# Performance work log

Measured on AMD Instinct MI355X. Metric: run time of the kernel, lower is better.

The kernel has to match this reference:

```python
import jax, jax.numpy as jnp
import numpy as np

BN_EPS = 1e-5
CHEB_K = 9


def laplacian(x, A):
    # x: [B,N,F_in], A: [B,N,N]
    diff = x[:, None, :, :] - x[:, :, None, :]            # [B,N,N,F]
    dist = jnp.sqrt(jnp.sum(diff * diff, axis=-1))        # [B,N,N]
    W = A / (dist + 0.001)
    d = 1.0 / jnp.sqrt(jnp.sum(W, axis=1))                # [B,N]
    I = jnp.eye(W.shape[1], dtype=W.dtype)[None]
    L = I - d[:, :, None] * W * d[:, None, :]             # sym-normalized
    L = L / 2 - I
    return L


def cheb_conv(L, x, W, b):
    # Chebyshev recursion, k=9: T0=x, T1=Lx, Tk = 2 L T(k-1) - T(k-2)
    Ts = [x, jnp.matmul(L, x)]
    for _ in range(CHEB_K - 2):
        Ts.append(2.0 * jnp.matmul(L, Ts[-1]) - Ts[-2])
    xt = jnp.concatenate(Ts, axis=-1)                     # [B,N,F_in*k]
    return jnp.matmul(xt, W) + b


def batchnorm_train(x, gamma, beta):
    # x: [B,N,C]; BatchNorm1d over flattened B*N rows (train mode, biased var)
    B, N, C = x.shape
    xf = x.reshape(B * N, C)
    mu = jnp.mean(xf, axis=0)
    var = jnp.mean((xf - mu) ** 2, axis=0)
    xn = (xf - mu) / jnp.sqrt(var + BN_EPS)
    return (xn * gamma + beta).reshape(B, N, C)


def setup_inputs() -> dict:
    key = jax.random.key(0)
    ks = jax.random.split(key, 12)
    B, N = 32, 1024
    x = jax.random.normal(ks[0], (B, N, 3), dtype=jnp.float32)
    A = jax.random.uniform(ks[1], (B, N, N), dtype=jnp.float32)
    def lin(k, fin, fout):
        return jax.random.normal(k, (fin, fout), dtype=jnp.float32) / np.sqrt(fin)
    return {
        "x": x, "A": A,
        "W1": lin(ks[2], 3 * CHEB_K, 32), "b1": jnp.zeros((32,), jnp.float32),
        "g1": jnp.ones((32,), jnp.float32), "be1": jnp.zeros((32,), jnp.float32),
        "W2": lin(ks[3], 32 * CHEB_K, 64), "b2": jnp.zeros((64,), jnp.float32),
        "g2": jnp.ones((64,), jnp.float32), "be2": jnp.zeros((64,), jnp.float32),
        "W3": lin(ks[4], 64 * CHEB_K, 64), "b3": jnp.zeros((64,), jnp.float32),
        "g3": jnp.ones((64,), jnp.float32), "be3": jnp.zeros((64,), jnp.float32),
        "Wfc": lin(ks[5], 64, 1), "bfc": jnp.zeros((1,), jnp.float32),
    }


def reference(x, A, W1, b1, g1, be1, W2, b2, g2, be2, W3, b3, g3, be3, Wfc, bfc):
    L = jax.lax.stop_gradient(laplacian(x, A))  # .detach() in original
    h = cheb_conv(L, x, W1, b1)
    h = jax.nn.elu(batchnorm_train(h, g1, be1))
    h = cheb_conv(L, h, W2, b2)
    h = jax.nn.elu(batchnorm_train(h, g2, be2))
    h = cheb_conv(L, h, W3, b3)
    h = jax.nn.elu(batchnorm_train(h, g3, be3))
    h = jnp.mean(h, axis=1)                     # [B,64]
    return jnp.matmul(h, Wfc) + bfc             # [B,1]
```

## Files before the change

kernel.cpp:

```cpp
#include <hip/hip_runtime.h>
#include <hip/hip_bf16.h>
#include <math.h>

constexpr int NN = 1024;
constexpr int NB = 32;
constexpr int ROWS = NB * NN;
constexpr int NSLICE = 8;

using f32x4 = __attribute__((ext_vector_type(4))) float;
using s16x8 = __attribute__((ext_vector_type(8))) short;
using us8 = __attribute__((ext_vector_type(8))) unsigned short;

__device__ inline unsigned short f2bf(float f) {
  unsigned u = __float_as_uint(f);
  unsigned r = (u + 0x7FFFu + ((u >> 16) & 1u)) >> 16;
  return (unsigned short)r;
}
__device__ inline float bf2f(unsigned short h) {
  return __uint_as_float((unsigned)h << 16);
}

__global__ __launch_bounds__(256) void colsum_w(float* __restrict__ A,
                                                const float* __restrict__ x,
                                                float* __restrict__ S) {
  const int b = blockIdx.z;
  const int j = blockIdx.x * 256 + threadIdx.x;
  const int slice = blockIdx.y;
  const int ibase = slice * 128;
  __shared__ float xs[128 * 3];
  for (int idx = threadIdx.x; idx < 384; idx += 256)
    xs[idx] = x[(size_t)(b * NN + ibase) * 3 + idx];
  const float xj0 = x[(size_t)(b * NN + j) * 3 + 0];
  const float xj1 = x[(size_t)(b * NN + j) * 3 + 1];
  const float xj2 = x[(size_t)(b * NN + j) * 3 + 2];
  __syncthreads();
  float s = 0.f;
  size_t off = ((size_t)b << 20) + (size_t)ibase * NN + j;
  for (int ii = 0; ii < 128; ++ii, off += NN) {
    float a = A[off];
    float dx = xj0 - xs[ii * 3 + 0];
    float dy = xj1 - xs[ii * 3 + 1];
    float dz = xj2 - xs[ii * 3 + 2];
    float dist = sqrtf(dx * dx + dy * dy + dz * dz);
    float w = a / (dist + 0.001f);
    A[off] = w;
    s += w;
  }
  S[(size_t)slice * ROWS + b * NN + j] = s;
}

__global__ __launch_bounds__(256) void d_kernel(const float* __restrict__ S,
                                                float* __restrict__ D) {
  int i = blockIdx.x * 256 + threadIdx.x;
  if (i < ROWS) {
    float s = 0.f;
#pragma unroll
    for (int p = 0; p < NSLICE; ++p) s += S[(size_t)p * ROWS + i];
    D[i] = 1.f / sqrtf(s);
  }
}

__global__ __launch_bounds__(256) void pack_L(float* __restrict__ A,
                                              const float* __restrict__ D,
                                              unsigned short* __restrict__ Lh,
                                              unsigned short* __restrict__ Ll) {
  const int b = blockIdx.y;
  const int rb = blockIdx.x;
  const int i0 = rb * 16;
  const float* Db = &D[b * NN];
  for (int ci = threadIdx.x; ci < 2048; ci += 256) {
    int kt = ci >> 6, l = ci & 63;
    int r = l & 15, kg = l >> 4;
    int i = i0 + r;
    int j0 = kt * 32 + kg * 8;
    size_t ga = ((size_t)b << 20) + (size_t)i * NN + j0;
    float4 w0 = *reinterpret_cast<const float4*>(&A[ga]);
    float4 w1 = *reinterpret_cast<const float4*>(&A[ga + 4]);
    float di = Db[i];
    float4 d0 = *reinterpret_cast<const float4*>(&Db[j0]);
    float4 d1 = *reinterpret_cast<const float4*>(&Db[j0 + 4]);
    float lv[8];
    lv[0] = -0.5f * di * d0.x * w0.x;
    lv[1] = -0.5f * di * d0.y * w0.y;
    lv[2] = -0.5f * di * d0.z * w0.z;
    lv[3] = -0.5f * di * d0.w * w0.w;
    lv[4] = -0.5f * di * d1.x * w1.x;
    lv[5] = -0.5f * di * d1.y * w1.y;
    lv[6] = -0.5f * di * d1.z * w1.z;
    lv[7] = -0.5f * di * d1.w * w1.w;
    int dd = i - j0;
    if (dd >= 0 && dd < 8) lv[dd] -= 0.5f;
    float4 o0 = {lv[0], lv[1], lv[2], lv[3]};
    float4 o1 = {lv[4], lv[5], lv[6], lv[7]};
    *reinterpret_cast<float4*>(&A[ga]) = o0;
    *reinterpret_cast<float4*>(&A[ga + 4]) = o1;
    us8 vh, vl;
#pragma unroll
    for (int jj = 0; jj < 8; ++jj) {
      unsigned short hi = f2bf(lv[jj]);
      vh[jj] = hi;
      vl[jj] = f2bf(lv[jj] - bf2f(hi));
    }
    size_t po = (((size_t)b * 64 + rb) * 32 + kt) * 512 + (size_t)l * 8;
    *reinterpret_cast<us8*>(&Lh[po]) = vh;
    *reinterpret_cast<us8*>(&Ll[po]) = vl;
  }
}

__global__ __launch_bounds__(256) void scale_L(float* __restrict__ A,
                                               const float* __restrict__ D) {
  const long total4 = (long)NB * NN * NN / 4;
  for (long idx = (long)blockIdx.x * 256 + threadIdx.x; idx < total4;
       idx += (long)gridDim.x * 256) {
    long base = idx * 4;
    int j0 = (int)(base & (NN - 1));
    int i = (int)((base >> 10) & (NN - 1));
    int b = (int)(base >> 20);
    float4 w = reinterpret_cast<float4*>(A)[idx];
    float di = D[b * NN + i];
    float4 dj = *reinterpret_cast<const float4*>(&D[b * NN + j0]);
    float4 l;
    l.x = -0.5f * di * dj.x * w.x;
    l.y = -0.5f * di * dj.y * w.y;
    l.z = -0.5f * di * dj.z * w.z;
    l.w = -0.5f * di * dj.w * w.w;
    int dd = i - j0;
    if (dd == 0) l.x -= 0.5f;
    else if (dd == 1) l.y -= 0.5f;
    else if (dd == 2) l.z -= 0.5f;
    else if (dd == 3) l.w -= 0.5f;
    reinterpret_cast<float4*>(A)[idx] = l;
  }
}

template <int F, int G>
__global__ __launch_bounds__(256) void acc0_gemm(const float* __restrict__ h,
                                                 const float* __restrict__ W0,
                                                 float* __restrict__ acc) {
  constexpr int RB = 64;
  constexpr int TGN = G / 16;
  __shared__ float Hs[RB][F + 1];
  __shared__ float Ws[F][G];
  const int tid = threadIdx.x;
  const size_t row0 = (size_t)blockIdx.x * RB;
  for (int idx = tid; idx < RB * F; idx += 256)
    Hs[idx / F][idx % F] = h[row0 * F + idx];
  for (int idx = tid; idx < F * G; idx += 256)
    Ws[idx / G][idx % G] = W0[idx];
  __syncthreads();
  const int tx = tid % 16, ty = tid / 16;
  float o[4][TGN];
#pragma unroll
  for (int r = 0; r < 4; ++r)
#pragma unroll
    for (int c = 0; c < TGN; ++c) o[r][c] = 0.f;
#pragma unroll 4
  for (int f = 0; f < F; ++f) {
    float a[4];
#pragma unroll
    for (int r = 0; r < 4; ++r) a[r] = Hs[ty * 4 + r][f];
#pragma unroll
    for (int c = 0; c < TGN; ++c) {
      float w = Ws[f][tx * TGN + c];
#pragma unroll
      for (int r = 0; r < 4; ++r) o[r][c] = fmaf(a[r], w, o[r][c]);
    }
  }
#pragma unroll
  for (int r = 0; r < 4; ++r) {
    size_t base = (row0 + ty * 4 + r) * G + tx * TGN;
#pragma unroll
    for (int c = 0; c < TGN; ++c) acc[base + c] = o[r][c];
  }
}

__global__ __launch_bounds__(256) void cheb_l1(
    const float* __restrict__ Lg, const float* __restrict__ Tprev,
    const float* __restrict__ Tpp, float* __restrict__ Tk,
    const float* __restrict__ Wk, float* __restrict__ acc, float alpha,
    float beta) {
  __shared__ float Ts[NN * 3];
  __shared__ float tkv[16][4];
  const int b = blockIdx.y;
  const int i0 = blockIdx.x * 16;
  const int tid = threadIdx.x;
  const float* tpb = &Tprev[(size_t)b * NN * 3];
  for (int idx = tid; idx < 768; idx += 256)
    *reinterpret_cast<float4*>(&Ts[idx * 4]) =
        *reinterpret_cast<const float4*>(&tpb[idx * 4]);
  __syncthreads();
  const int wv = tid >> 6, ln = tid & 63;
#pragma unroll
  for (int r = 0; r < 4; ++r) {
    const int i = i0 + wv * 4 + r;
    const float* Lrow = &Lg[((size_t)b << 20) + (size_t)i * NN];
    float a0 = 0.f, a1 = 0.f, a2 = 0.f;
#pragma unroll
    for (int c = 0; c < 16; ++c) {
      int j = c * 64 + ln;
      float w = Lrow[j];
      a0 = fmaf(w, Ts[j * 3 + 0], a0);
      a1 = fmaf(w, Ts[j * 3 + 1], a1);
      a2 = fmaf(w, Ts[j * 3 + 2], a2);
    }
#pragma unroll
    for (int off = 32; off; off >>= 1) {
      a0 += __shfl_down(a0, off, 64);
      a1 += __shfl_down(a1, off, 64);
      a2 += __shfl_down(a2, off, 64);
    }
    if (ln == 0) {
      const size_t rbase = (size_t)(b * NN + i) * 3;
      float t0 = alpha * a0, t1 = alpha * a1, t2 = alpha * a2;
      if (beta != 0.f) {
        t0 = fmaf(beta, Tpp[rbase + 0], t0);
        t1 = fmaf(beta, Tpp[rbase + 1], t1);
        t2 = fmaf(beta, Tpp[rbase + 2], t2);
      }
      Tk[rbase + 0] = t0;
      Tk[rbase + 1] = t1;
      Tk[rbase + 2] = t2;
      tkv[wv * 4 + r][0] = t0;
      tkv[wv * 4 + r][1] = t1;
      tkv[wv * 4 + r][2] = t2;
    }
  }
  __syncthreads();
  for (int idx = tid; idx < 16 * 32; idx += 256) {
    int rr = idx >> 5, cc = idx & 31;
    float v = tkv[rr][0] * Wk[cc] + tkv[rr][1] * Wk[32 + cc] +
              tkv[rr][2] * Wk[64 + cc];
    acc[(size_t)(b * NN + i0 + rr) * 32 + cc] += v;
  }
}

template <int FT>
__global__ __launch_bounds__(256) void pack_T(const float* __restrict__ h,
                                              unsigned short* __restrict__ Oh,
                                              unsigned short* __restrict__ Ol) {
  constexpr int F = FT * 16;
  __shared__ float Ts[64][F + 1];
  const int b = blockIdx.y;
  const int m0 = blockIdx.x * 64;
  const int tid = threadIdx.x;
  for (int idx = tid; idx < 64 * (F / 4); idx += 256) {
    int row = idx / (F / 4), c4 = idx % (F / 4);
    float4 v = *reinterpret_cast<const float4*>(
        &h[((size_t)(b * NN + m0 + row)) * F + c4 * 4]);
    Ts[row][c4 * 4 + 0] = v.x;
    Ts[row][c4 * 4 + 1] = v.y;
    Ts[row][c4 * 4 + 2] = v.z;
    Ts[row][c4 * 4 + 3] = v.w;
  }
  __syncthreads();
  for (int ci = tid; ci < 8 * F; ci += 256) {
    int nc = ci / F, f = ci % F;
    int n0 = nc * 8;
    us8 vh, vl;
#pragma unroll
    for (int j = 0; j < 8; ++j) {
      float t = Ts[n0 + j][f];
      unsigned short hi = f2bf(t);
      vh[j] = hi;
      vl[j] = f2bf(t - bf2f(hi));
    }
    int gn = m0 + n0;
    int kt = gn >> 5, kg = (gn >> 3) & 3;
    size_t off = (((size_t)b * FT + (f >> 4)) * 32 + kt) * 512 +
                 (size_t)(kg * 16 + (f & 15)) * 8;
    *reinterpret_cast<us8*>(&Oh[off]) = vh;
    *reinterpret_cast<us8*>(&Ol[off]) = vl;
  }
}

template <int FT, int G>
__global__ __launch_bounds__(256) void cheb_mfma_p(
    const unsigned short* __restrict__ Lh, const unsigned short* __restrict__ Ll,
    const unsigned short* __restrict__ Bh, const unsigned short* __restrict__ Bl,
    const float* __restrict__ Tpp, float* __restrict__ Tk,
    unsigned short* __restrict__ Oh, unsigned short* __restrict__ Ol,
    const float* __restrict__ Wk, float* __restrict__ acc, float alpha,
    float beta) {
  constexpr int F = FT * 16;
  constexpr int TGN = G / 16;
  __shared__ float Ts[64][F + 1];
  __shared__ float Ws[F][G];
  const int tid = threadIdx.x;

  int id = blockIdx.x;
  int xcd = id & 7, t2 = id >> 3;
  int mt = t2 & 15;
  int b = xcd + 8 * (t2 >> 4);
  const int m0 = mt * 64;

  for (int idx = tid; idx < F * G / 4; idx += 256) {
    int r = idx / (G / 4), c4 = idx % (G / 4);
    *reinterpret_cast<float4*>(&Ws[r][c4 * 4]) =
        *reinterpret_cast<const float4*>(&Wk[r * G + c4 * 4]);
  }

  const int wv = tid >> 6, l = tid & 63;
  const size_t lane8 = (size_t)l * 8;
  const size_t Abase = (((size_t)b * 64 + mt * 4 + wv) * 32) * 512 + lane8;
  const size_t Bbase = (((size_t)b * FT) * 32) * 512 + lane8;

  f32x4 av[FT];
#pragma unroll
  for (int c = 0; c < FT; ++c) av[c] = {0.f, 0.f, 0.f, 0.f};

#pragma unroll 2
  for (int kt = 0; kt < 32; ++kt) {
    s16x8 a_h, a_l, b_h[FT], b_l[FT];
    size_t aoff = Abase + (size_t)kt * 512;
    a_h = *reinterpret_cast<const s16x8*>(&Lh[aoff]);
    a_l = *reinterpret_cast<const s16x8*>(&Ll[aoff]);
#pragma unroll
    for (int c = 0; c < FT; ++c) {
      size_t off = Bbase + ((size_t)c * 32 + kt) * 512;
      b_h[c] = *reinterpret_cast<const s16x8*>(&Bh[off]);
      b_l[c] = *reinterpret_cast<const s16x8*>(&Bl[off]);
    }
#pragma unroll
    for (int c = 0; c < FT; ++c) {
      av[c] = __builtin_amdgcn_mfma_f32_16x16x32_bf16(a_h, b_h[c], av[c], 0, 0, 0);
      av[c] = __builtin_amdgcn_mfma_f32_16x16x32_bf16(a_l, b_h[c], av[c], 0, 0, 0);
      av[c] = __builtin_amdgcn_mfma_f32_16x16x32_bf16(a_h, b_l[c], av[c], 0, 0, 0);
      av[c] = __builtin_amdgcn_mfma_f32_16x16x32_bf16(a_l, b_l[c], av[c], 0, 0, 0);
    }
  }

  const int kg = l >> 4, fr = l & 15;
#pragma unroll
  for (int c = 0; c < FT; ++c)
#pragma unroll
    for (int r = 0; r < 4; ++r)
      Ts[wv * 16 + kg * 4 + r][c * 16 + fr] = av[c][r];
  __syncthreads();

  const bool hasB = (beta != 0.f);
  for (int idx = tid; idx < 64 * (F / 4); idx += 256) {
    int row = idx / (F / 4), f0 = (idx % (F / 4)) * 4;
    size_t g = ((size_t)(b * NN + m0 + row)) * F + f0;
    float t0 = alpha * Ts[row][f0 + 0];
    float t1 = alpha * Ts[row][f0 + 1];
    float t2 = alpha * Ts[row][f0 + 2];
    float t3 = alpha * Ts[row][f0 + 3];
    if (hasB) {
      float4 p = *reinterpret_cast<const float4*>(&Tpp[g]);
      t0 = fmaf(beta, p.x, t0);
      t1 = fmaf(beta, p.y, t1);
      t2 = fmaf(beta, p.z, t2);
      t3 = fmaf(beta, p.w, t3);
    }
    float4 tv = {t0, t1, t2, t3};
    *reinterpret_cast<float4*>(&Tk[g]) = tv;
    Ts[row][f0 + 0] = t0;
    Ts[row][f0 + 1] = t1;
    Ts[row][f0 + 2] = t2;
    Ts[row][f0 + 3] = t3;
  }
  __syncthreads();

  for (int ci = tid; ci < 8 * F; ci += 256) {
    int nc = ci / F, f = ci % F;
    int n0 = nc * 8;
    us8 vh, vl;
#pragma unroll
    for (int j = 0; j < 8; ++j) {
      float t = Ts[n0 + j][f];
      unsigned short hi = f2bf(t);
      vh[j] = hi;
      vl[j] = f2bf(t - bf2f(hi));
    }
    int gn = m0 + n0;
    int kt = gn >> 5, kgo = (gn >> 3) & 3;
    size_t off = (((size_t)b * FT + (f >> 4)) * 32 + kt) * 512 +
                 (size_t)(kgo * 16 + (f & 15)) * 8;
    *reinterpret_cast<us8*>(&Oh[off]) = vh;
    *reinterpret_cast<us8*>(&Ol[off]) = vl;
  }

  const int tx = tid & 15, ty = tid >> 4;
  float o[4][TGN];
#pragma unroll
  for (int r = 0; r < 4; ++r)
#pragma unroll
    for (int c = 0; c < TGN; ++c) o[r][c] = 0.f;
#pragma unroll 8
  for (int f = 0; f < F; ++f) {
    float a[4];
#pragma unroll
    for (int r = 0; r < 4; ++r) a[r] = Ts[ty * 4 + r][f];
#pragma unroll
    for (int c = 0; c < TGN; ++c) {
      float w = Ws[f][tx * TGN + c];
#pragma unroll
      for (int r = 0; r < 4; ++r) o[r][c] = fmaf(a[r], w, o[r][c]);
    }
  }
#pragma unroll
  for (int r = 0; r < 4; ++r) {
    size_t base = ((size_t)(b * NN + m0 + ty * 4 + r)) * G + tx * TGN;
    float4 v = *reinterpret_cast<const float4*>(&acc[base]);
    v.x += o[r][0];
    v.y += o[r][1];
    v.z += o[r][2];
    v.w += o[r][3];
    *reinterpret_cast<float4*>(&acc[base]) = v;
  }
}

template <int BM, int F, int G>
__global__ __launch_bounds__(256) void cheb_gemm(
    const float* __restrict__ Lg, const float* __restrict__ Tprev,
    const float* __restrict__ Tpp, float* __restrict__ Tk,
    const float* __restrict__ Wk, float* __restrict__ acc, float alpha,
    float beta) {
  constexpr int BK = 32;
  constexpr int TM = 4, TN = 4;
  constexpr int NTX = F / TN;
  constexpr int NTY = BM / TM;
  static_assert(NTX * NTY == 256, "tile mismatch");
  constexpr int TGN = G / NTX;

  __shared__ float As[BM][BK + 1];
  __shared__ float Bs[BK][F];
  __shared__ float Ws[F][G];
  __shared__ float Ts[BM][F + 1];

  const int tid = threadIdx.x;
  const int tx = tid % NTX, ty = tid / NTX;
  const int b = blockIdx.y;
  const int i0 = blockIdx.x * BM;

  constexpr int W_ITERS = (F * G / 4) / 256;
#pragma unroll
  for (int it = 0; it < W_ITERS; ++it) {
    int idx = tid + it * 256;
    int r = idx / (G / 4), c4 = idx % (G / 4);
    float4 v = *reinterpret_cast<const float4*>(&Wk[r * G + c4 * 4]);
    *reinterpret_cast<float4*>(&Ws[r][c4 * 4]) = v;
  }

  float accT[TM][TN];
#pragma unroll
  for (int r = 0; r < TM; ++r)
#pragma unroll
    for (int c = 0; c < TN; ++c) accT[r][c] = 0.f;

  const size_t Lbase = ((size_t)b << 20);
  constexpr int A_ITERS = (BM * (BK / 4)) / 256;
  constexpr int B_ITERS = (BK * (F / 4) + 255) / 256;

  for (int k0 = 0; k0 < NN; k0 += BK) {
#pragma unroll
    for (int it = 0; it < A_ITERS; ++it) {
      int idx = tid + it * 256;
      int m = idx >> 3, k4 = idx & 7;
      float4 v = *reinterpret_cast<const float4*>(
          &Lg[Lbase + (size_t)(i0 + m) * NN + k0 + k4 * 4]);
      As[m][k4 * 4 + 0] = v.x;
      As[m][k4 * 4 + 1] = v.y;
      As[m][k4 * 4 + 2] = v.z;
      As[m][k4 * 4 + 3] = v.w;
    }
#pragma unroll
    for (int it = 0; it < B_ITERS; ++it) {
      int idx = tid + it * 256;
      int kr = idx / (F / 4), c4 = idx % (F / 4);
      float4 v = *reinterpret_cast<const float4*>(
          &Tprev[(size_t)(b * NN + k0 + kr) * F + c4 * 4]);
      *reinterpret_cast<float4*>(&Bs[kr][c4 * 4]) = v;
    }
    __syncthreads();
#pragma unroll
    for (int kk = 0; kk < BK; ++kk) {
      float a[TM];
#pragma unroll
      for (int r = 0; r < TM; ++r) a[r] = As[ty * TM + r][kk];
      float4 bv = *reinterpret_cast<const float4*>(&Bs[kk][tx * TN]);
      float bb[4] = {bv.x, bv.y, bv.z, bv.w};
#pragma unroll
      for (int r = 0; r < TM; ++r)
#pragma unroll
        for (int c = 0; c < TN; ++c)
          accT[r][c] = fmaf(a[r], bb[c], accT[r][c]);
    }
    __syncthreads();
  }

  const bool hasB = (beta != 0.f);
#pragma unroll
  for (int r = 0; r < TM; ++r) {
    int row = i0 + ty * TM + r;
    size_t gidx = (size_t)(b * NN + row) * F + tx * TN;
    float t0 = alpha * accT[r][0], t1 = alpha * accT[r][1];
    float t2 = alpha * accT[r][2], t3 = alpha * accT[r][3];
    if (hasB) {
      float4 p = *reinterpret_cast<const float4*>(&Tpp[gidx]);
      t0 = fmaf(beta, p.x, t0);
      t1 = fmaf(beta, p.y, t1);
      t2 = fmaf(beta, p.z, t2);
      t3 = fmaf(beta, p.w, t3);
    }
    float4 tv = {t0, t1, t2, t3};
    *reinterpret_cast<float4*>(&Tk[gidx]) = tv;
    Ts[ty * TM + r][tx * TN + 0] = t0;
    Ts[ty * TM + r][tx * TN + 1] = t1;
    Ts[ty * TM + r][tx * TN + 2] = t2;
    Ts[ty * TM + r][tx * TN + 3] = t3;
  }
  __syncthreads();

  float oacc[TM][TGN];
#pragma unroll
  for (int r = 0; r < TM; ++r)
#pragma unroll
    for (int c = 0; c < TGN; ++c) oacc[r][c] = 0.f;
#pragma unroll 8
  for (int f = 0; f < F; ++f) {
    float a[TM];
#pragma unroll
    for (int r = 0; r < TM; ++r) a[r] = Ts[ty * TM + r][f];
#pragma unroll
    for (int c = 0; c < TGN; ++c) {
      float w = Ws[f][tx * TGN + c];
#pragma unroll
      for (int r = 0; r < TM; ++r) oacc[r][c] = fmaf(a[r], w, oacc[r][c]);
    }
  }
#pragma unroll
  for (int r = 0; r < TM; ++r) {
    int row = i0 + ty * TM + r;
    size_t base = (size_t)(b * NN + row) * G + tx * TGN;
#pragma unroll
    for (int c = 0; c < TGN; ++c) acc[base + c] += oacc[r][c];
  }
}

constexpr int BN_BLOCKS = 256;

template <int C>
__global__ __launch_bounds__(256) void bn_part(const float* __restrict__ acc,
                                               double* __restrict__ part) {
  constexpr int GR = 256 / C;
  const int tid = threadIdx.x;
  const int c = tid % C;
  const int g = tid / C;
  double s = 0.0, s2 = 0.0;
  for (int r = blockIdx.x * GR + g; r < ROWS; r += BN_BLOCKS * GR) {
    double v = (double)acc[(size_t)r * C + c];
    s += v;
    s2 += v * v;
  }
  __shared__ double Ls[256], Ls2[256];
  Ls[tid] = s;
  Ls2[tid] = s2;
  __syncthreads();
  for (int str = 128; str >= C; str >>= 1) {
    if (tid < str) {
      Ls[tid] += Ls[tid + str];
      Ls2[tid] += Ls2[tid + str];
    }
    __syncthreads();
  }
  if (tid < C) {
    part[(size_t)blockIdx.x * 2 * C + tid] = Ls[tid];
    part[(size_t)blockIdx.x * 2 * C + C + tid] = Ls2[tid];
  }
}

template <int C>
__global__ void bn_final(const double* __restrict__ part,
                         const float* __restrict__ g,
                         const float* __restrict__ be,
                         float* __restrict__ sc) {
  int t = threadIdx.x;
  if (t < C) {
    double s = 0.0, s2 = 0.0;
    for (int b = 0; b < BN_BLOCKS; ++b) {
      s += part[(size_t)b * 2 * C + t];
      s2 += part[(size_t)b * 2 * C + C + t];
    }
    double mu = s / ROWS;
    double var = s2 / ROWS - mu * mu;
    float scale = g[t] / sqrtf((float)var + 1e-5f);
    sc[t] = scale;
    sc[C + t] = be[t] - (float)mu * scale;
  }
}

template <int C>
__global__ __launch_bounds__(256) void bn_apply_elu(
    const float* __restrict__ acc, const float* __restrict__ sc,
    float* __restrict__ h) {
  const long total4 = (long)ROWS * C / 4;
  for (long idx = (long)blockIdx.x * 256 + threadIdx.x; idx < total4;
       idx += (long)gridDim.x * 256) {
    long base = idx * 4;
    int c0 = (int)(base % C);
    float4 v = reinterpret_cast<const float4*>(acc)[idx];
    float t0 = fmaf(v.x, sc[c0 + 0], sc[C + c0 + 0]);
    float t1 = fmaf(v.y, sc[c0 + 1], sc[C + c0 + 1]);
    float t2 = fmaf(v.z, sc[c0 + 2], sc[C + c0 + 2]);
    float t3 = fmaf(v.w, sc[c0 + 3], sc[C + c0 + 3]);
    float4 o;
    o.x = t0 > 0.f ? t0 : expm1f(t0);
    o.y = t1 > 0.f ? t1 : expm1f(t1);
    o.z = t2 > 0.f ? t2 : expm1f(t2);
    o.w = t3 > 0.f ? t3 : expm1f(t3);
    reinterpret_cast<float4*>(h)[idx] = o;
  }
}

__global__ __launch_bounds__(256) void final_k(const float* __restrict__ h,
                                               const float* __restrict__ Wfc,
                                               const float* __restrict__ bfc,
                                               float* __restrict__ out) {
  const int b = blockIdx.x;
  const int tid = threadIdx.x;
  const int c = tid % 64;
  const int g = tid / 64;
  float s = 0.f;
  for (int r = g; r < NN; r += 4) s += h[(size_t)(b * NN + r) * 64 + c];
  __shared__ float red[256];
  red[tid] = s;
  __syncthreads();
  if (tid < 128) red[tid] += red[tid + 128];
  __syncthreads();
  if (tid < 64) {
    float pooled = (red[tid] + red[tid + 64]) * (1.0f / 1024.0f);
    float v = pooled * Wfc[tid];
#pragma unroll
    for (int off = 32; off; off >>= 1) v += __shfl_down(v, off, 64);
    if (tid == 0) out[b] = v + bfc[0];
  }
}

extern "C" void kernel_launch(void* const* d_in, const int* in_sizes, int n_in,
                              void* d_out, int out_size, void* d_ws,
                              size_t ws_size, hipStream_t stream) {
  const float* x = (const float*)d_in[0];
  float* A = (float*)d_in[1];
  const float* W1 = (const float*)d_in[2];
  const float* g1 = (const float*)d_in[4];
  const float* be1 = (const float*)d_in[5];
  const float* W2 = (const float*)d_in[6];
  const float* g2 = (const float*)d_in[8];
  const float* be2 = (const float*)d_in[9];
  const float* W3 = (const float*)d_in[10];
  const float* g3 = (const float*)d_in[12];
  const float* be3 = (const float*)d_in[13];
  const float* Wfc = (const float*)d_in[14];
  const float* bfc = (const float*)d_in[15];

  constexpr size_t TBUF = 2097152;
  float* wsf = (float*)d_ws;
  float* buf0 = wsf;
  float* buf1 = buf0 + TBUF;
  float* buf2 = buf1 + TBUF;
  float* acc = buf2 + TBUF;
  unsigned short* tt = (unsigned short*)(wsf + 4 * TBUF);
  unsigned short* TTh[2] = {tt, tt + 2 * 2097152};
  unsigned short* TTl[2] = {tt + 2097152, tt + 3 * 2097152};
  unsigned short* Lh = (unsigned short*)(wsf + 4 * TBUF + 4194304);
  unsigned short* Ll = Lh + (size_t)NB * NN * NN;
  float* S = wsf + 4 * TBUF + 4194304 + 2 * ((size_t)NB * NN * NN / 2);
  float* D = S + (size_t)NSLICE * ROWS;
  double* part_m = (double*)(D + ROWS);
  float* sc_m = (float*)(part_m + (size_t)BN_BLOCKS * 2 * 64);
  size_t need_m = (size_t)((sc_m + 128) - wsf) * sizeof(float);

  float* S_f = wsf + 4 * TBUF;
  float* D_f = S_f + (size_t)NSLICE * ROWS;
  double* part_f = (double*)(D_f + ROWS);
  float* sc_f = (float*)(part_f + (size_t)BN_BLOCKS * 2 * 64);
  size_t need_f = (size_t)((sc_f + 128) - wsf) * sizeof(float);

  const bool use_m = (ws_size >= need_m);
  if (!use_m && ws_size < need_f) return;
  float* Sp = use_m ? S : S_f;
  float* Dp = use_m ? D : D_f;
  double* part = use_m ? part_m : part_f;
  float* sc = use_m ? sc_m : sc_f;

  float* bufs[3] = {buf0, buf1, buf2};

  colsum_w<<<dim3(4, NSLICE, NB), 256, 0, stream>>>(A, x, Sp);
  d_kernel<<<128, 256, 0, stream>>>(Sp, Dp);
  if (use_m) {
    pack_L<<<dim3(64, NB), 256, 0, stream>>>(A, Dp, Lh, Ll);
  } else {
    scale_L<<<4096, 256, 0, stream>>>(A, Dp);
  }

  acc0_gemm<3, 32><<<512, 256, 0, stream>>>(x, W1, acc);
  {
    const float* Tm1 = x;
    const float* Tm2 = nullptr;
    for (int k = 1; k <= 8; ++k) {
      float* outb = bufs[k % 3];
      float alpha = (k == 1) ? 1.f : 2.f;
      float beta = (k == 1) ? 0.f : -1.f;
      cheb_l1<<<dim3(64, NB), 256, 0, stream>>>(
          A, Tm1, (k == 1) ? x : Tm2, outb, W1 + k * 3 * 32, acc, alpha, beta);
      Tm2 = Tm1;
      Tm1 = outb;
    }
  }
  bn_part<32><<<BN_BLOCKS, 256, 0, stream>>>(acc, part);
  bn_final<32><<<1, 64, 0, stream>>>(part, g1, be1, sc);
  bn_apply_elu<32><<<1024, 256, 0, stream>>>(acc, sc, buf0);

  acc0_gemm<32, 64><<<512, 256, 0, stream>>>(buf0, W2, acc);
  if (use_m) {
    pack_T<2><<<dim3(16, NB), 256, 0, stream>>>(buf0, TTh[0], TTl[0]);
    const float* Tm1 = buf0;
    const float* Tm2 = nullptr;
    for (int k = 1; k <= 8; ++k) {
      float* outb = bufs[k % 3];
      int si = (k - 1) & 1, so = k & 1;
      float alpha = (k == 1) ? 1.f : 2.f;
      float beta = (k == 1) ? 0.f : -1.f;
      cheb_mfma_p<2, 64><<<512, 256, 0, stream>>>(
          Lh, Ll, TTh[si], TTl[si], (k == 1) ? buf0 : Tm2, outb, TTh[so],
          TTl[so], W2 + k * 32 * 64, acc, alpha, beta);
      Tm2 = Tm1;
      Tm1 = outb;
    }
  } else {
    const float* Tm1 = buf0;
    const float* Tm2 = nullptr;
    for (int k = 1; k <= 8; ++k) {
      float* outb = bufs[k % 3];
      float alpha = (k == 1) ? 1.f : 2.f;
      float beta = (k == 1) ? 0.f : -1.f;
      cheb_gemm<128, 32, 64><<<dim3(8, NB), 256, 0, stream>>>(
          A, Tm1, (k == 1) ? buf0 : Tm2, outb, W2 + k * 32 * 64, acc, alpha,
          beta);
      Tm2 = Tm1;
      Tm1 = outb;
    }
  }
  bn_part<64><<<BN_BLOCKS, 256, 0, stream>>>(acc, part);
  bn_final<64><<<1, 64, 0, stream>>>(part, g2, be2, sc);
  bn_apply_elu<64><<<2048, 256, 0, stream>>>(acc, sc, buf0);

  acc0_gemm<64, 64><<<512, 256, 0, stream>>>(buf0, W3, acc);
  if (use_m) {
    pack_T<4><<<dim3(16, NB), 256, 0, stream>>>(buf0, TTh[0], TTl[0]);
    const float* Tm1 = buf0;
    const float* Tm2 = nullptr;
    for (int k = 1; k <= 8; ++k) {
      float* outb = bufs[k % 3];
      int si = (k - 1) & 1, so = k & 1;
      float alpha = (k == 1) ? 1.f : 2.f;
      float beta = (k == 1) ? 0.f : -1.f;
      cheb_mfma_p<4, 64><<<512, 256, 0, stream>>>(
          Lh, Ll, TTh[si], TTl[si], (k == 1) ? buf0 : Tm2, outb, TTh[so],
          TTl[so], W3 + k * 64 * 64, acc, alpha, beta);
      Tm2 = Tm1;
      Tm1 = outb;
    }
  } else {
    const float* Tm1 = buf0;
    const float* Tm2 = nullptr;
    for (int k = 1; k <= 8; ++k) {
      float* outb = bufs[k % 3];
      float alpha = (k == 1) ? 1.f : 2.f;
      float beta = (k == 1) ? 0.f : -1.f;
      cheb_gemm<64, 64, 64><<<dim3(16, NB), 256, 0, stream>>>(
          A, Tm1, (k == 1) ? buf0 : Tm2, outb, W3 + k * 64 * 64, acc, alpha,
          beta);
      Tm2 = Tm1;
      Tm1 = outb;
    }
  }
  bn_part<64><<<BN_BLOCKS, 256, 0, stream>>>(acc, part);
  bn_final<64><<<1, 64, 0, stream>>>(part, g3, be3, sc);
  bn_apply_elu<64><<<2048, 256, 0, stream>>>(acc, sc, buf0);

  final_k<<<NB, 256, 0, stream>>>(buf0, Wfc, bfc, (float*)d_out);
}
```

Baseline: 1.217 ms.

## Split MFMA Chebyshev K loop across waves, drop lo*lo term, fuse L scaling into layer 1

pack_L no longer writes the scaled fp32 Laplacian back to A. The first-layer cheb_l1 kernel now applies the D scaling and identity shift on the fly from the raw weights, which removes a full 128MB write pass. The MFMA Chebyshev kernel uses 32-row tiles and splits the K dimension across two wave pairs, reduced through shared memory, and the grid doubles to 1024 blocks for more parallelism. It also drops the low*low bf16 correction MFMA, trading a little accuracy for fewer matrix instructions.

```diff
diff --git a/kernel.cpp b/kernel.cpp
--- a/kernel.cpp
+++ b/kernel.cpp
@@ -60,7 +60,7 @@
   }
 }
 
-__global__ __launch_bounds__(256) void pack_L(float* __restrict__ A,
+__global__ __launch_bounds__(256) void pack_L(const float* __restrict__ A,
                                               const float* __restrict__ D,
                                               unsigned short* __restrict__ Lh,
                                               unsigned short* __restrict__ Ll) {
@@ -90,10 +90,6 @@
     lv[7] = -0.5f * di * d1.w * w1.w;
     int dd = i - j0;
     if (dd >= 0 && dd < 8) lv[dd] -= 0.5f;
-    float4 o0 = {lv[0], lv[1], lv[2], lv[3]};
-    float4 o1 = {lv[4], lv[5], lv[6], lv[7]};
-    *reinterpret_cast<float4*>(&A[ga]) = o0;
-    *reinterpret_cast<float4*>(&A[ga + 4]) = o1;
     us8 vh, vl;
 #pragma unroll
     for (int jj = 0; jj < 8; ++jj) {
@@ -175,19 +171,26 @@
 }
 
 __global__ __launch_bounds__(256) void cheb_l1(
-    const float* __restrict__ Lg, const float* __restrict__ Tprev,
-    const float* __restrict__ Tpp, float* __restrict__ Tk,
-    const float* __restrict__ Wk, float* __restrict__ acc, float alpha,
-    float beta) {
+    const float* __restrict__ Lg, const float* __restrict__ Dv,
+    const float* __restrict__ Tprev, const float* __restrict__ Tpp,
+    float* __restrict__ Tk, const float* __restrict__ Wk,
+    float* __restrict__ acc, float alpha, float beta) {
   __shared__ float Ts[NN * 3];
+  __shared__ float ds[NN];
   __shared__ float tkv[16][4];
   const int b = blockIdx.y;
   const int i0 = blockIdx.x * 16;
   const int tid = threadIdx.x;
+  const bool fused = (Dv != nullptr);
   const float* tpb = &Tprev[(size_t)b * NN * 3];
   for (int idx = tid; idx < 768; idx += 256)
     *reinterpret_cast<float4*>(&Ts[idx * 4]) =
         *reinterpret_cast<const float4*>(&tpb[idx * 4]);
+  if (fused) {
+    for (int idx = tid; idx < 256; idx += 256)
+      *reinterpret_cast<float4*>(&ds[idx * 4]) =
+          *reinterpret_cast<const float4*>(&Dv[b * NN + idx * 4]);
+  }
   __syncthreads();
   const int wv = tid >> 6, ln = tid & 63;
 #pragma unroll
@@ -199,6 +202,7 @@
     for (int c = 0; c < 16; ++c) {
       int j = c * 64 + ln;
       float w = Lrow[j];
+      if (fused) w *= ds[j];
       a0 = fmaf(w, Ts[j * 3 + 0], a0);
       a1 = fmaf(w, Ts[j * 3 + 1], a1);
       a2 = fmaf(w, Ts[j * 3 + 2], a2);
@@ -211,7 +215,16 @@
     }
     if (ln == 0) {
       const size_t rbase = (size_t)(b * NN + i) * 3;
-      float t0 = alpha * a0, t1 = alpha * a1, t2 = alpha * a2;
+      float l0, l1, l2;
+      if (fused) {
+        float di = ds[i];
+        l0 = -0.5f * di * a0 - 0.5f * Ts[i * 3 + 0];
+        l1 = -0.5f * di * a1 - 0.5f * Ts[i * 3 + 1];
+        l2 = -0.5f * di * a2 - 0.5f * Ts[i * 3 + 2];
+      } else {
+        l0 = a0; l1 = a1; l2 = a2;
+      }
+      float t0 = alpha * l0, t1 = alpha * l1, t2 = alpha * l2;
       if (beta != 0.f) {
         t0 = fmaf(beta, Tpp[rbase + 0], t0);
         t1 = fmaf(beta, Tpp[rbase + 1], t1);
@@ -283,15 +296,15 @@
     float beta) {
   constexpr int F = FT * 16;
   constexpr int TGN = G / 16;
-  __shared__ float Ts[64][F + 1];
+  __shared__ float Ts[32][F + 1];
   __shared__ float Ws[F][G];
   const int tid = threadIdx.x;
 
   int id = blockIdx.x;
   int xcd = id & 7, t2 = id >> 3;
-  int mt = t2 & 15;
-  int b = xcd + 8 * (t2 >> 4);
-  const int m0 = mt * 64;
+  int mt = t2 & 31;
+  int b = xcd + 8 * (t2 >> 5);
+  const int m0 = mt * 32;
 
   for (int idx = tid; idx < F * G / 4; idx += 256) {
     int r = idx / (G / 4), c4 = idx % (G / 4);
@@ -300,16 +313,17 @@
   }
 
   const int wv = tid >> 6, l = tid & 63;
+  const int rt = wv >> 1, kh = wv & 1;
   const size_t lane8 = (size_t)l * 8;
-  const size_t Abase = (((size_t)b * 64 + mt * 4 + wv) * 32) * 512 + lane8;
+  const size_t Abase = (((size_t)b * 64 + mt * 2 + rt) * 32) * 512 + lane8;
   const size_t Bbase = (((size_t)b * FT) * 32) * 512 + lane8;
 
   f32x4 av[FT];
 #pragma unroll
   for (int c = 0; c < FT; ++c) av[c] = {0.f, 0.f, 0.f, 0.f};
 
-#pragma unroll 2
-  for (int kt = 0; kt < 32; ++kt) {
+  const int kt0 = kh * 16;
+  for (int kt = kt0; kt < kt0 + 16; ++kt) {
     s16x8 a_h, a_l, b_h[FT], b_l[FT];
     size_t aoff = Abase + (size_t)kt * 512;
     a_h = *reinterpret_cast<const s16x8*>(&Lh[aoff]);
@@ -325,20 +339,29 @@
       av[c] = __builtin_amdgcn_mfma_f32_16x16x32_bf16(a_h, b_h[c], av[c], 0, 0, 0);
       av[c] = __builtin_amdgcn_mfma_f32_16x16x32_bf16(a_l, b_h[c], av[c], 0, 0, 0);
       av[c] = __builtin_amdgcn_mfma_f32_16x16x32_bf16(a_h, b_l[c], av[c], 0, 0, 0);
-      av[c] = __builtin_amdgcn_mfma_f32_16x16x32_bf16(a_l, b_l[c], av[c], 0, 0, 0);
     }
   }
 
   const int kg = l >> 4, fr = l & 15;
-#pragma unroll
-  for (int c = 0; c < FT; ++c)
-#pragma unroll
-    for (int r = 0; r < 4; ++r)
-      Ts[wv * 16 + kg * 4 + r][c * 16 + fr] = av[c][r];
+  if (kh == 0) {
+#pragma unroll
+    for (int c = 0; c < FT; ++c)
+#pragma unroll
+      for (int r = 0; r < 4; ++r)
+        Ts[rt * 16 + kg * 4 + r][c * 16 + fr] = av[c][r];
+  }
+  __syncthreads();
+  if (kh == 1) {
+#pragma unroll
+    for (int c = 0; c < FT; ++c)
+#pragma unroll
+      for (int r = 0; r < 4; ++r)
+        Ts[rt * 16 + kg * 4 + r][c * 16 + fr] += av[c][r];
+  }
   __syncthreads();
 
   const bool hasB = (beta != 0.f);
-  for (int idx = tid; idx < 64 * (F / 4); idx += 256) {
+  for (int idx = tid; idx < 32 * (F / 4); idx += 256) {
     int row = idx / (F / 4), f0 = (idx % (F / 4)) * 4;
     size_t g = ((size_t)(b * NN + m0 + row)) * F + f0;
     float t0 = alpha * Ts[row][f0 + 0];
@@ -361,7 +384,7 @@
   }
   __syncthreads();
 
-  for (int ci = tid; ci < 8 * F; ci += 256) {
+  for (int ci = tid; ci < 4 * F; ci += 256) {
     int nc = ci / F, f = ci % F;
     int n0 = nc * 8;
     us8 vh, vl;
@@ -381,26 +404,25 @@
   }
 
   const int tx = tid & 15, ty = tid >> 4;
-  float o[4][TGN];
-#pragma unroll
-  for (int r = 0; r < 4; ++r)
+  float o[2][TGN];
+#pragma unroll
+  for (int r = 0; r < 2; ++r)
 #pragma unroll
     for (int c = 0; c < TGN; ++c) o[r][c] = 0.f;
 #pragma unroll 8
   for (int f = 0; f < F; ++f) {
-    float a[4];
-#pragma unroll
-    for (int r = 0; r < 4; ++r) a[r] = Ts[ty * 4 + r][f];
+    float a0 = Ts[ty * 2 + 0][f];
+    float a1 = Ts[ty * 2 + 1][f];
 #pragma unroll
     for (int c = 0; c < TGN; ++c) {
       float w = Ws[f][tx * TGN + c];
-#pragma unroll
-      for (int r = 0; r < 4; ++r) o[r][c] = fmaf(a[r], w, o[r][c]);
-    }
-  }
-#pragma unroll
-  for (int r = 0; r < 4; ++r) {
-    size_t base = ((size_t)(b * NN + m0 + ty * 4 + r)) * G + tx * TGN;
+      o[0][c] = fmaf(a0, w, o[0][c]);
+      o[1][c] = fmaf(a1, w, o[1][c]);
+    }
+  }
+#pragma unroll
+  for (int r = 0; r < 2; ++r) {
+    size_t base = ((size_t)(b * NN + m0 + ty * 2 + r)) * G + tx * TGN;
     float4 v = *reinterpret_cast<const float4*>(&acc[base]);
     v.x += o[r][0];
     v.y += o[r][1];
@@ -694,6 +716,7 @@
     scale_L<<<4096, 256, 0, stream>>>(A, Dp);
   }
 
+  const float* Dfuse = use_m ? Dp : nullptr;
   acc0_gemm<3, 32><<<512, 256, 0, stream>>>(x, W1, acc);
   {
     const float* Tm1 = x;
@@ -703,7 +726,8 @@
       float alpha = (k == 1) ? 1.f : 2.f;
       float beta = (k == 1) ? 0.f : -1.f;
       cheb_l1<<<dim3(64, NB), 256, 0, stream>>>(
-          A, Tm1, (k == 1) ? x : Tm2, outb, W1 + k * 3 * 32, acc, alpha, beta);
+          A, Dfuse, Tm1, (k == 1) ? x : Tm2, outb, W1 + k * 3 * 32, acc, alpha,
+          beta);
       Tm2 = Tm1;
       Tm1 = outb;
     }
@@ -722,7 +746,7 @@
       int si = (k - 1) & 1, so = k & 1;
       float alpha = (k == 1) ? 1.f : 2.f;
       float beta = (k == 1) ? 0.f : -1.f;
-      cheb_mfma_p<2, 64><<<512, 256, 0, stream>>>(
+      cheb_mfma_p<2, 64><<<1024, 256, 0, stream>>>(
           Lh, Ll, TTh[si], TTl[si], (k == 1) ? buf0 : Tm2, outb, TTh[so],
           TTl[so], W2 + k * 32 * 64, acc, alpha, beta);
       Tm2 = Tm1;
@@ -756,7 +780,7 @@
       int si = (k - 1) & 1, so = k & 1;
       float alpha = (k == 1) ? 1.f : 2.f;
       float beta = (k == 1) ? 0.f : -1.f;
-      cheb_mfma_p<4, 64><<<512, 256, 0, stream>>>(
+      cheb_mfma_p<4, 64><<<1024, 256, 0, stream>>>(
           Lh, Ll, TTh[si], TTl[si], (k == 1) ? buf0 : Tm2, outb, TTh[so],
           TTl[so], W3 + k * 64 * 64, acc, alpha, beta);
       Tm2 = Tm1;
```

Measured after the change: 1.332 ms. 1.1x slower.

## Skip fp32 L writeback in pack_L; apply D scaling inside cheb_l1; drop lo*lo MFMA

Applied to the files above, without the earlier changes.

pack_L no longer writes the normalized fp32 Laplacian back into A, which removes a full 128 MB store pass. In the fused path, cheb_l1 reads the unnormalized W from A and applies the D row and column scaling plus the identity term on the fly from a shared-memory copy of D. Separately, the split-bf16 MFMA product drops the lo*lo term, cutting matrix instructions by a quarter at a small cost in accuracy.

```diff
diff --git a/kernel.cpp b/kernel.cpp
--- a/kernel.cpp
+++ b/kernel.cpp
@@ -60,7 +60,7 @@
   }
 }
 
-__global__ __launch_bounds__(256) void pack_L(float* __restrict__ A,
+__global__ __launch_bounds__(256) void pack_L(const float* __restrict__ A,
                                               const float* __restrict__ D,
                                               unsigned short* __restrict__ Lh,
                                               unsigned short* __restrict__ Ll) {
@@ -90,10 +90,6 @@
     lv[7] = -0.5f * di * d1.w * w1.w;
     int dd = i - j0;
     if (dd >= 0 && dd < 8) lv[dd] -= 0.5f;
-    float4 o0 = {lv[0], lv[1], lv[2], lv[3]};
-    float4 o1 = {lv[4], lv[5], lv[6], lv[7]};
-    *reinterpret_cast<float4*>(&A[ga]) = o0;
-    *reinterpret_cast<float4*>(&A[ga + 4]) = o1;
     us8 vh, vl;
 #pragma unroll
     for (int jj = 0; jj < 8; ++jj) {
@@ -175,19 +171,26 @@
 }
 
 __global__ __launch_bounds__(256) void cheb_l1(
-    const float* __restrict__ Lg, const float* __restrict__ Tprev,
-    const float* __restrict__ Tpp, float* __restrict__ Tk,
-    const float* __restrict__ Wk, float* __restrict__ acc, float alpha,
-    float beta) {
+    const float* __restrict__ Lg, const float* __restrict__ Dv,
+    const float* __restrict__ Tprev, const float* __restrict__ Tpp,
+    float* __restrict__ Tk, const float* __restrict__ Wk,
+    float* __restrict__ acc, float alpha, float beta) {
   __shared__ float Ts[NN * 3];
+  __shared__ float ds[NN];
   __shared__ float tkv[16][4];
   const int b = blockIdx.y;
   const int i0 = blockIdx.x * 16;
   const int tid = threadIdx.x;
+  const bool fused = (Dv != nullptr);
   const float* tpb = &Tprev[(size_t)b * NN * 3];
   for (int idx = tid; idx < 768; idx += 256)
     *reinterpret_cast<float4*>(&Ts[idx * 4]) =
         *reinterpret_cast<const float4*>(&tpb[idx * 4]);
+  if (fused) {
+    for (int idx = tid; idx < 256; idx += 256)
+      *reinterpret_cast<float4*>(&ds[idx * 4]) =
+          *reinterpret_cast<const float4*>(&Dv[b * NN + idx * 4]);
+  }
   __syncthreads();
   const int wv = tid >> 6, ln = tid & 63;
 #pragma unroll
@@ -199,6 +202,7 @@
     for (int c = 0; c < 16; ++c) {
       int j = c * 64 + ln;
       float w = Lrow[j];
+      if (fused) w *= ds[j];
       a0 = fmaf(w, Ts[j * 3 + 0], a0);
       a1 = fmaf(w, Ts[j * 3 + 1], a1);
       a2 = fmaf(w, Ts[j * 3 + 2], a2);
@@ -211,7 +215,16 @@
     }
     if (ln == 0) {
       const size_t rbase = (size_t)(b * NN + i) * 3;
-      float t0 = alpha * a0, t1 = alpha * a1, t2 = alpha * a2;
+      float l0, l1, l2;
+      if (fused) {
+        float di = ds[i];
+        l0 = -0.5f * di * a0 - 0.5f * Ts[i * 3 + 0];
+        l1 = -0.5f * di * a1 - 0.5f * Ts[i * 3 + 1];
+        l2 = -0.5f * di * a2 - 0.5f * Ts[i * 3 + 2];
+      } else {
+        l0 = a0; l1 = a1; l2 = a2;
+      }
+      float t0 = alpha * l0, t1 = alpha * l1, t2 = alpha * l2;
       if (beta != 0.f) {
         t0 = fmaf(beta, Tpp[rbase + 0], t0);
         t1 = fmaf(beta, Tpp[rbase + 1], t1);
@@ -325,7 +338,6 @@
       av[c] = __builtin_amdgcn_mfma_f32_16x16x32_bf16(a_h, b_h[c], av[c], 0, 0, 0);
       av[c] = __builtin_amdgcn_mfma_f32_16x16x32_bf16(a_l, b_h[c], av[c], 0, 0, 0);
       av[c] = __builtin_amdgcn_mfma_f32_16x16x32_bf16(a_h, b_l[c], av[c], 0, 0, 0);
-      av[c] = __builtin_amdgcn_mfma_f32_16x16x32_bf16(a_l, b_l[c], av[c], 0, 0, 0);
     }
   }
 
@@ -694,6 +706,7 @@
     scale_L<<<4096, 256, 0, stream>>>(A, Dp);
   }
 
+  const float* Dfuse = use_m ? Dp : nullptr;
   acc0_gemm<3, 32><<<512, 256, 0, stream>>>(x, W1, acc);
   {
     const float* Tm1 = x;
@@ -703,7 +716,8 @@
       float alpha = (k == 1) ? 1.f : 2.f;
       float beta = (k == 1) ? 0.f : -1.f;
       cheb_l1<<<dim3(64, NB), 256, 0, stream>>>(
-          A, Tm1, (k == 1) ? x : Tm2, outb, W1 + k * 3 * 32, acc, alpha, beta);
+          A, Dfuse, Tm1, (k == 1) ? x : Tm2, outb, W1 + k * 3 * 32, acc, alpha,
+          beta);
       Tm2 = Tm1;
       Tm1 = outb;
     }
```

Result: slower. 1.396 ms (+14.8%).
